# Performance work log

Hardware: AMD Instinct MI355X
Metric: run time of the kernel (lower is better)

The kernel has to match this reference:

```python
import jax, jax.numpy as jnp
import numpy as np

B, L, D, H = 4, 2048, 1024, 16
HD = D // H
EPS = 1e-5


def _layernorm(x, g, b):
    mu = jnp.mean(x, axis=-1, keepdims=True)
    var = jnp.mean(jnp.square(x - mu), axis=-1, keepdims=True)
    return (x - mu) * jax.lax.rsqrt(var + EPS) * g + b


def _rotate_half(x):
    x1, x2 = jnp.split(x, 2, axis=-1)
    return jnp.concatenate([-x2, x1], axis=-1)


def setup_inputs() -> dict:
    key = jax.random.key(0)
    ks = jax.random.split(key, 12)
    s = 0.02
    return {
        "x": jax.random.normal(ks[0], (B, L, D), jnp.float32),
        "pos_cos": jax.random.uniform(ks[1], (B, L, D), jnp.float32),
        "pos_sin": jax.random.uniform(ks[2], (B, L, D), jnp.float32),
        "attn_mask": jnp.zeros((B, L), jnp.float32),
        "Wq": jax.random.normal(ks[3], (D, D), jnp.float32) * s,
        "Wk": jax.random.normal(ks[4], (D, D), jnp.float32) * s,
        "Wv": jax.random.normal(ks[5], (D, D), jnp.float32) * s,
        "Wo": jax.random.normal(ks[6], (D, D), jnp.float32) * s,
        "W1": jax.random.normal(ks[7], (D, 2 * D), jnp.float32) * s,
        "W2": jax.random.normal(ks[8], (D, D), jnp.float32) * s,
        "g1": jnp.ones((D,), jnp.float32),
        "b1": jnp.zeros((D,), jnp.float32),
        "g2": jnp.ones((D,), jnp.float32),
        "b2": jnp.zeros((D,), jnp.float32),
    }


def reference(x, pos_cos, pos_sin, attn_mask, Wq, Wk, Wv, Wo, W1, W2, g1, b1, g2, b2):
    # --- attention sublayer (pre-LN) ---
    residual = x
    xn = _layernorm(x, g1, b1)
    split_heads = lambda t: t.reshape(B, L, H, HD).transpose(0, 2, 1, 3)  # [B,H,L,hd]
    q = split_heads(xn @ Wq)
    k = split_heads(xn @ Wk)
    v = split_heads(xn @ Wv)
    cos = split_heads(pos_cos)
    sin = split_heads(pos_sin)
    q = q * cos + _rotate_half(q) * sin
    k = k * cos + _rotate_half(k) * sin
    scores = jnp.einsum('bhqd,bhkd->bhqk', q, k) / np.float32(np.sqrt(HD))
    scores = scores + attn_mask[:, None, None, :]  # additive mask over keys
    probs = jax.nn.softmax(scores, axis=-1)
    ctx = jnp.einsum('bhqk,bhkd->bhqd', probs, v)
    ctx = ctx.transpose(0, 2, 1, 3).reshape(B, L, D)
    x = residual + ctx @ Wo
    # --- SwiGLU FFN sublayer (pre-LN) ---
    residual = x
    xn = _layernorm(x, g2, b2)
    h = xn @ W1
    x1, x2 = h[..., :D], h[..., D:]
    ffn = (jax.nn.silu(x1) * x2) @ W2
    return residual + ffn
```

## Files before the change

kernel.cpp:

```cpp
#include <hip/hip_runtime.h>
#include <hip/hip_bf16.h>

typedef unsigned short ushort_t;
typedef short short8 __attribute__((ext_vector_type(8)));
typedef unsigned short u16x4 __attribute__((ext_vector_type(4)));
typedef float f32x4 __attribute__((ext_vector_type(4)));
typedef int int2v __attribute__((ext_vector_type(2)));
typedef int int4v __attribute__((ext_vector_type(4)));

#define MFMA_BF16 __builtin_amdgcn_mfma_f32_16x16x32_bf16

#define GLDS16(g, l) __builtin_amdgcn_global_load_lds( \
    (__attribute__((address_space(1))) void*)(g), \
    (__attribute__((address_space(3))) void*)(l), 16, 0, 0)

__device__ __forceinline__ unsigned short f2bf(float f) {
  union { float f; unsigned u; } v; v.f = f;
  unsigned r = v.u + 0x7FFFu + ((v.u >> 16) & 1u);
  return (unsigned short)(r >> 16);
}
__device__ __forceinline__ float bf2f(unsigned short h) {
  union { unsigned u; float f; } v; v.u = ((unsigned)h) << 16;
  return v.f;
}
__device__ __forceinline__ unsigned pack_bf2(float a, float b) {
  __hip_bfloat162 t = __float22bfloat162_rn(float2{a, b});
  union { __hip_bfloat162 h; unsigned u; } v; v.h = t;
  return v.u;
}
__device__ __forceinline__ float exp2_raw(float x) {
  float r;
  asm volatile("v_exp_f32 %0, %1" : "=v"(r) : "v"(x));
  return r;
}

#define BB 4
#define LL 2048
#define DD 1024
#define HH 16
#define HD 64
#define NROW (BB * LL)
#define LOG2E 1.4426950408889634f

template <int PERM>
__global__ __launch_bounds__(256) void wconv(const float* __restrict__ W,
                                             ushort_t* __restrict__ WT,
                                             int R, int C) {
  __shared__ float tile[32][33];
  const int ct = blockIdx.x * 32, rt = blockIdx.y * 32;
  const int tx = threadIdx.x & 31, ty = threadIdx.x >> 5;
#pragma unroll
  for (int j = 0; j < 4; ++j)
    tile[ty + j * 8][tx] = W[(size_t)(rt + ty + j * 8) * C + ct + tx];
  __syncthreads();
  int orow0 = ct;
  if (PERM)
    orow0 = (ct < 1024) ? ((ct >> 5) * 64) : ((((ct - 1024) >> 5) * 64) + 32);
#pragma unroll
  for (int j = 0; j < 4; ++j)
    WT[(size_t)(orow0 + ty + j * 8) * R + rt + tx] = f2bf(tile[tx][ty + j * 8]);
}

__global__ void mask_scale(const float* __restrict__ mask,
                           float* __restrict__ maskl) {
  const int i = blockIdx.x * 256 + threadIdx.x;
  maskl[i] = mask[i] * LOG2E;
}

template <int BIN>
__global__ __launch_bounds__(256) void ln_kernel(const void* __restrict__ xin,
                                                 const float* __restrict__ g,
                                                 const float* __restrict__ bt,
                                                 ushort_t* __restrict__ out,
                                                 ushort_t* __restrict__ xb) {
  const int row = blockIdx.x, t = threadIdx.x;
  f32x4 v;
  if (BIN) {
    const u16x4 hv =
        *(const u16x4*)((const ushort_t*)xin + (size_t)row * DD + t * 4);
    v[0] = bf2f(hv[0]); v[1] = bf2f(hv[1]);
    v[2] = bf2f(hv[2]); v[3] = bf2f(hv[3]);
  } else {
    v = *(const f32x4*)((const float*)xin + (size_t)row * DD + t * 4);
    if (xb) {
      u16x4 xo;
      xo[0] = f2bf(v[0]); xo[1] = f2bf(v[1]);
      xo[2] = f2bf(v[2]); xo[3] = f2bf(v[3]);
      *(u16x4*)(xb + (size_t)row * DD + t * 4) = xo;
    }
  }
  float s = v[0] + v[1] + v[2] + v[3];
  float sq = v[0] * v[0] + v[1] * v[1] + v[2] * v[2] + v[3] * v[3];
#pragma unroll
  for (int off = 1; off < 64; off <<= 1) {
    s += __shfl_xor(s, off);
    sq += __shfl_xor(sq, off);
  }
  __shared__ float aw[4], aq[4];
  if ((t & 63) == 0) { aw[t >> 6] = s; aq[t >> 6] = sq; }
  __syncthreads();
  s = aw[0] + aw[1] + aw[2] + aw[3];
  sq = aq[0] + aq[1] + aq[2] + aq[3];
  const float mu = s * (1.f / DD);
  const float var = sq * (1.f / DD) - mu * mu;
  const float rs = rsqrtf(var + 1e-5f);
  u16x4 o;
#pragma unroll
  for (int j = 0; j < 4; ++j) {
    const int c = t * 4 + j;
    o[j] = f2bf((v[j] - mu) * rs * g[c] + bt[c]);
  }
  *(u16x4*)(out + (size_t)row * DD + t * 4) = o;
}

template <int EPI>
__global__ __launch_bounds__(256) void gemm64(
    const ushort_t* __restrict__ A, const ushort_t* __restrict__ BT,
    const float* __restrict__ pcos, const float* __restrict__ psin,
    ushort_t* __restrict__ qh, ushort_t* __restrict__ kh,
    ushort_t* __restrict__ vt, ushort_t* __restrict__ gact,
    ushort_t* __restrict__ Cb, float* __restrict__ Cf,
    const ushort_t* __restrict__ residb,
    int M, int N, int K) {
  __shared__ ushort_t As[128 * 64];
  __shared__ ushort_t Bs[128 * 64];
  const int tid = threadIdx.x;
  const int lane = tid & 63;
  const int w = tid >> 6;
  const int wr = w >> 1, wc = w & 1;
  const int orig = blockIdx.y * gridDim.x + blockIdx.x;
  const int xcd = orig & 7;
  const int lid = orig >> 3;
  const int bm = (xcd * 8 + (lid & 7)) * 128;
  const int bn = (lid >> 3) * 128;
  const int fr = lane & 15;
  const int hi = lane >> 4;
  const int srow8 = lane >> 3;
  const int schunk = (lane & 7) ^ srow8;
  f32x4 acc[4][4];
#pragma unroll
  for (int m = 0; m < 4; ++m)
#pragma unroll
    for (int n = 0; n < 4; ++n) acc[m][n] = (f32x4){0.f, 0.f, 0.f, 0.f};

  const int nk = K >> 6;
  for (int kt = 0; kt < nk; ++kt) {
    __syncthreads();
#pragma unroll
    for (int c = 0; c < 4; ++c) {
      const int rbase = w * 32 + c * 8;
      const int grow = rbase + srow8;
      GLDS16(A + (size_t)(bm + grow) * K + kt * 64 + schunk * 8,
             &As[rbase * 64]);
      GLDS16(BT + (size_t)(bn + grow) * K + kt * 64 + schunk * 8,
             &Bs[rbase * 64]);
    }
    asm volatile("s_waitcnt vmcnt(0)" ::: "memory");
    __syncthreads();
#pragma unroll
    for (int khf = 0; khf < 2; ++khf) {
      short8 af[4], bf_[4];
#pragma unroll
      for (int m = 0; m < 4; ++m) {
        const int r = wr * 64 + m * 16 + fr;
        af[m] = *(const short8*)&As[r * 64 + (((khf << 2) + hi) ^ (fr & 7)) * 8];
      }
#pragma unroll
      for (int n = 0; n < 4; ++n) {
        const int r = wc * 64 + n * 16 + fr;
        bf_[n] = *(const short8*)&Bs[r * 64 + (((khf << 2) + hi) ^ (fr & 7)) * 8];
      }
#pragma unroll
      for (int m = 0; m < 4; ++m)
#pragma unroll
        for (int n = 0; n < 4; ++n)
          acc[m][n] = MFMA_BF16(af[m], bf_[n], acc[m][n], 0, 0, 0);
    }
  }

  if (EPI == 1) {
    const int gcol = bn + wc * 64;
    const int region = gcol >> 10;
    const int h = (gcol & 1023) >> 6;
    const int b = bm >> 11;
    if (region < 2) {
      const float qs = (region == 0) ? (0.125f * LOG2E) : 1.0f;
      ushort_t* dstbuf = (region == 0) ? qh : kh;
      const int dbase = h * 64;
#pragma unroll
      for (int m = 0; m < 4; ++m) {
        const int gr0 = bm + wr * 64 + m * 16 + hi * 4;
#pragma unroll
        for (int r = 0; r < 4; ++r) {
          const int gr = gr0 + r;
          const int l = gr & 2047;
          const float* pcr = pcos + (size_t)gr * DD + dbase;
          const float* psr = psin + (size_t)gr * DD + dbase;
          ushort_t* dst = dstbuf + ((size_t)(b * HH + h) * LL + l) * HD;
#pragma unroll
          for (int n = 0; n < 2; ++n) {
            const int dlo = n * 16 + fr;
            const float xlo = acc[m][n][r], xhi = acc[m][n + 2][r];
            dst[dlo] = f2bf((xlo * pcr[dlo] - xhi * psr[dlo]) * qs);
            dst[dlo + 32] = f2bf((xhi * pcr[dlo + 32] + xlo * psr[dlo + 32]) * qs);
          }
        }
      }
    } else {
      const size_t bhv = (size_t)(b * HH + h);
      const int l0 = (bm & 2047) + wr * 64;
      const int lt = l0 >> 6;
#pragma unroll
      for (int m = 0; m < 4; ++m) {
        const int slotb = 32 * (m >> 1) + 8 * hi + 4 * (m & 1);
#pragma unroll
        for (int n = 0; n < 4; ++n) {
          const int hd = n * 16 + fr;
          u16x4 wv;
          wv[0] = f2bf(acc[m][n][0]);
          wv[1] = f2bf(acc[m][n][1]);
          wv[2] = f2bf(acc[m][n][2]);
          wv[3] = f2bf(acc[m][n][3]);
          *(u16x4*)(vt + (bhv * HD + hd) * LL + lt * 64 + slotb) = wv;
        }
      }
    }
  } else if (EPI == 2) {
    const int jbase = ((bn + wc * 64) >> 6) * 32;
#pragma unroll
    for (int m = 0; m < 4; ++m) {
      const int gr0 = bm + wr * 64 + m * 16 + hi * 4;
#pragma unroll
      for (int r = 0; r < 4; ++r) {
        ushort_t* dst = gact + (size_t)(gr0 + r) * DD + jbase;
#pragma unroll
        for (int n = 0; n < 2; ++n) {
          const float x1 = acc[m][n][r];
          const float x2 = acc[m][n + 2][r];
          dst[n * 16 + fr] = f2bf(x1 / (1.f + __expf(-x1)) * x2);
        }
      }
    }
  } else {
#pragma unroll
    for (int m = 0; m < 4; ++m)
#pragma unroll
      for (int n = 0; n < 4; ++n)
#pragma unroll
        for (int r = 0; r < 4; ++r) {
          const int gr = bm + wr * 64 + m * 16 + hi * 4 + r;
          const int gc = bn + wc * 64 + n * 16 + fr;
          const size_t o = (size_t)gr * N + gc;
          if (EPI == 3) Cb[o] = f2bf(bf2f(residb[o]) + acc[m][n][r]);
          else          Cf[o] = bf2f(residb[o]) + acc[m][n][r];
        }
  }
}

__global__ __launch_bounds__(512) void attn_kernel(
    const ushort_t* __restrict__ qh, const ushort_t* __restrict__ kh,
    const ushort_t* __restrict__ vt, const float* __restrict__ maskl,
    ushort_t* __restrict__ ctx) {
  const int tid = threadIdx.x, lane = tid & 63, w = tid >> 6;
  const int flat = blockIdx.y * gridDim.x + blockIdx.x;
  const int xcd = flat & 7;
  const int slot = flat >> 3;
  const int bh = xcd * 8 + (slot >> 4);
  const int q0 = (slot & 15) * 128;
  const int b = bh >> 4, h = bh & 15;
  __shared__ ushort_t Ks[2][64 * 64];
  __shared__ ushort_t Vs[2][64 * 64];
  const int fr = lane & 15;
  const int hi = lane >> 4;
  const int fo = hi * 8;
  const int qrow = q0 + w * 16 + fr;
  const size_t qoff = ((size_t)bh * LL + qrow) * HD + fo;
  const short8 qf0 = *(const short8*)(qh + qoff);
  const short8 qf1 = *(const short8*)(qh + qoff + 32);
  short8 ones;
#pragma unroll
  for (int i = 0; i < 8; ++i) ones[i] = (short)0x3F80;

  f32x4 oacc[4];
  f32x4 lacc = (f32x4){0.f, 0.f, 0.f, 0.f};
#pragma unroll
  for (int m = 0; m < 4; ++m) oacc[m] = (f32x4){0.f, 0.f, 0.f, 0.f};

  const int lrow = lane >> 3;
  const int lcs = ((lane & 7) ^ lrow) * 8;
  const int rr = w * 8 + lrow;

  const float* mrow = maskl + (size_t)b * LL;

  const int NT = LL / 128;
  for (int kt = 0; kt < NT; ++kt) {
    __syncthreads();
    GLDS16(kh + ((size_t)bh * LL + kt * 128 + rr) * HD + lcs, &Ks[0][w * 512]);
    GLDS16(kh + ((size_t)bh * LL + kt * 128 + 64 + rr) * HD + lcs,
           &Ks[1][w * 512]);
    GLDS16(vt + ((size_t)bh * HD + rr) * LL + kt * 128 + lcs, &Vs[0][w * 512]);
    GLDS16(vt + ((size_t)bh * HD + rr) * LL + kt * 128 + 64 + lcs,
           &Vs[1][w * 512]);
    f32x4 mk[8];
#pragma unroll
    for (int n = 0; n < 8; ++n)
      mk[n] = *(const f32x4*)(mrow + kt * 128 + n * 16 + hi * 4);
    asm volatile("s_waitcnt vmcnt(0)" ::: "memory");
    __syncthreads();

#pragma unroll
    for (int sub = 0; sub < 2; ++sub) {
      f32x4 s[4];
#pragma unroll
      for (int n = 0; n < 4; ++n) s[n] = mk[sub * 4 + n];
      __builtin_amdgcn_s_setprio(1);
#pragma unroll
      for (int n = 0; n < 4; ++n) {
        const int krow = n * 16 + fr;
#pragma unroll
        for (int c = 0; c < 2; ++c) {
          const int col = (c * 32 + fo) ^ ((fr & 7) * 8);
          const short8 kf = *(const short8*)&Ks[sub][krow * 64 + col];
          s[n] = MFMA_BF16(kf, c ? qf1 : qf0, s[n], 0, 0, 0);
        }
      }
      __builtin_amdgcn_s_setprio(0);
      unsigned pk[4][2];
#pragma unroll
      for (int n = 0; n < 4; ++n) {
        const float p0 = exp2_raw(s[n][0]);
        const float p1 = exp2_raw(s[n][1]);
        const float p2 = exp2_raw(s[n][2]);
        const float p3 = exp2_raw(s[n][3]);
        pk[n][0] = pack_bf2(p0, p1);
        pk[n][1] = pack_bf2(p2, p3);
      }
      __builtin_amdgcn_s_setprio(1);
#pragma unroll
      for (int c = 0; c < 2; ++c) {
        int4v pw = {(int)pk[2 * c][0], (int)pk[2 * c][1],
                    (int)pk[2 * c + 1][0], (int)pk[2 * c + 1][1]};
        union { int4v i; short8 s; } pf; pf.i = pw;
#pragma unroll
        for (int m = 0; m < 4; ++m) {
          const int row = m * 16 + fr;
          const int col = (c * 32 + fo) ^ ((fr & 7) * 8);
          const short8 vf = *(const short8*)&Vs[sub][row * 64 + col];
          oacc[m] = MFMA_BF16(vf, pf.s, oacc[m], 0, 0, 0);
        }
        lacc = MFMA_BF16(ones, pf.s, lacc, 0, 0, 0);
      }
      __builtin_amdgcn_s_setprio(0);
    }
  }
  const float inv = 1.f / lacc[0];
  const int q = q0 + w * 16 + fr;
  ushort_t* dst = ctx + ((size_t)b * LL + q) * DD + h * 64 + hi * 4;
#pragma unroll
  for (int m = 0; m < 4; ++m) {
    int2v val;
    val[0] = (int)pack_bf2(oacc[m][0] * inv, oacc[m][1] * inv);
    val[1] = (int)pack_bf2(oacc[m][2] * inv, oacc[m][3] * inv);
    *(int2v*)(dst + m * 16) = val;
  }
}

extern "C" void kernel_launch(void* const* d_in, const int* in_sizes, int n_in,
                              void* d_out, int out_size, void* d_ws,
                              size_t ws_size, hipStream_t stream) {
  const float* x = (const float*)d_in[0];
  const float* pcos = (const float*)d_in[1];
  const float* psin = (const float*)d_in[2];
  const float* mask = (const float*)d_in[3];
  const float* Wq = (const float*)d_in[4];
  const float* Wk = (const float*)d_in[5];
  const float* Wv = (const float*)d_in[6];
  const float* Wo = (const float*)d_in[7];
  const float* W1 = (const float*)d_in[8];
  const float* W2 = (const float*)d_in[9];
  const float* g1 = (const float*)d_in[10];
  const float* b1 = (const float*)d_in[11];
  const float* g2 = (const float*)d_in[12];
  const float* b2 = (const float*)d_in[13];
  float* out = (float*)d_out;
  char* ws = (char*)d_ws;

  ushort_t* WQKVT = (ushort_t*)(ws);
  ushort_t* WOT = (ushort_t*)(ws + 6291456);
  ushort_t* W1T = (ushort_t*)(ws + 8388608);
  ushort_t* W2T = (ushort_t*)(ws + 12582912);
  ushort_t* XN = (ushort_t*)(ws + 14680064);
  float* MASKL = (float*)(ws + 31457280);
  ushort_t* XB = (ushort_t*)(ws + 31457280 + 1048576);
  ushort_t* GACT = (ushort_t*)(ws + 31457280 + 33554432);
  ushort_t* QH = (ushort_t*)(ws + 81788928);
  ushort_t* KH = (ushort_t*)(ws + 98566144);
  ushort_t* VT = (ushort_t*)(ws + 115343360);
  ushort_t* CTX = (ushort_t*)(ws + 132120576);
  ushort_t* XMIDB = (ushort_t*)(ws + 148897792);

  wconv<0><<<dim3(32, 32), 256, 0, stream>>>(Wq, WQKVT, 1024, 1024);
  wconv<0><<<dim3(32, 32), 256, 0, stream>>>(Wk, WQKVT + 1024 * 1024, 1024, 1024);
  wconv<0><<<dim3(32, 32), 256, 0, stream>>>(Wv, WQKVT + 2 * 1024 * 1024, 1024, 1024);
  wconv<0><<<dim3(32, 32), 256, 0, stream>>>(Wo, WOT, 1024, 1024);
  wconv<1><<<dim3(64, 32), 256, 0, stream>>>(W1, W1T, 1024, 2048);
  wconv<0><<<dim3(32, 32), 256, 0, stream>>>(W2, W2T, 1024, 1024);
  mask_scale<<<(BB * LL) / 256, 256, 0, stream>>>(mask, MASKL);

  ln_kernel<0><<<NROW, 256, 0, stream>>>(x, g1, b1, XN, XB);
  gemm64<1><<<dim3(24, 64), 256, 0, stream>>>(
      XN, WQKVT, pcos, psin, QH, KH, VT, nullptr, nullptr, nullptr, nullptr,
      NROW, 3072, 1024);
  attn_kernel<<<dim3(16, 64), 512, 0, stream>>>(QH, KH, VT, MASKL, CTX);
  gemm64<3><<<dim3(8, 64), 256, 0, stream>>>(
      CTX, WOT, nullptr, nullptr, nullptr, nullptr, nullptr, nullptr, XMIDB,
      nullptr, XB, NROW, 1024, 1024);
  ln_kernel<1><<<NROW, 256, 0, stream>>>(XMIDB, g2, b2, XN, nullptr);
  gemm64<2><<<dim3(16, 64), 256, 0, stream>>>(
      XN, W1T, nullptr, nullptr, nullptr, nullptr, nullptr, GACT, nullptr,
      nullptr, nullptr, NROW, 2048, 1024);
  gemm64<4><<<dim3(8, 64), 256, 0, stream>>>(
      GACT, W2T, nullptr, nullptr, nullptr, nullptr, nullptr, nullptr, nullptr,
      out, XMIDB, NROW, 1024, 1024);
}
```

Baseline: 333.5 us.

## Double-buffer LDS tiles in gemm64 to overlap global loads with MFMA

Splits the A/B shared-memory tiles into two buffers and issues the global-to-LDS loads for the next K tile before computing on the current one. A partial vmcnt wait lets the prefetch stay in flight while the current tile is consumed. It also raises wave priority around the MFMA block. This doubles LDS use per block to 64KB, which may lower occupancy, and adds a barrier at the end of each iteration.

```diff
diff --git a/kernel.cpp b/kernel.cpp
--- a/kernel.cpp
+++ b/kernel.cpp
@@ -122,8 +122,8 @@
     ushort_t* __restrict__ Cb, float* __restrict__ Cf,
     const ushort_t* __restrict__ residb,
     int M, int N, int K) {
-  __shared__ ushort_t As[128 * 64];
-  __shared__ ushort_t Bs[128 * 64];
+  __shared__ ushort_t As[2][128 * 64];
+  __shared__ ushort_t Bs[2][128 * 64];
   const int tid = threadIdx.x;
   const int lane = tid & 63;
   const int w = tid >> 6;
@@ -143,19 +143,29 @@
 #pragma unroll
     for (int n = 0; n < 4; ++n) acc[m][n] = (f32x4){0.f, 0.f, 0.f, 0.f};
 
+#define STAGE64(kt, bb)                                                      \
+  {                                                                          \
+    _Pragma("unroll") for (int c = 0; c < 4; ++c) {                          \
+      const int rbase = w * 32 + c * 8;                                      \
+      const int grow = rbase + srow8;                                        \
+      GLDS16(A + (size_t)(bm + grow) * K + (kt) * 64 + schunk * 8,           \
+             &As[bb][rbase * 64]);                                           \
+      GLDS16(BT + (size_t)(bn + grow) * K + (kt) * 64 + schunk * 8,          \
+             &Bs[bb][rbase * 64]);                                           \
+    }                                                                        \
+  }
+
   const int nk = K >> 6;
+  STAGE64(0, 0);
+#pragma unroll 1
   for (int kt = 0; kt < nk; ++kt) {
-    __syncthreads();
-#pragma unroll
-    for (int c = 0; c < 4; ++c) {
-      const int rbase = w * 32 + c * 8;
-      const int grow = rbase + srow8;
-      GLDS16(A + (size_t)(bm + grow) * K + kt * 64 + schunk * 8,
-             &As[rbase * 64]);
-      GLDS16(BT + (size_t)(bn + grow) * K + kt * 64 + schunk * 8,
-             &Bs[rbase * 64]);
-    }
-    asm volatile("s_waitcnt vmcnt(0)" ::: "memory");
+    const int cur = kt & 1;
+    if (kt + 1 < nk) {
+      STAGE64(kt + 1, cur ^ 1);
+      asm volatile("s_waitcnt vmcnt(8)" ::: "memory");
+    } else {
+      asm volatile("s_waitcnt vmcnt(0)" ::: "memory");
+    }
     __syncthreads();
 #pragma unroll
     for (int khf = 0; khf < 2; ++khf) {
@@ -163,20 +173,26 @@
 #pragma unroll
       for (int m = 0; m < 4; ++m) {
         const int r = wr * 64 + m * 16 + fr;
-        af[m] = *(const short8*)&As[r * 64 + (((khf << 2) + hi) ^ (fr & 7)) * 8];
+        af[m] =
+            *(const short8*)&As[cur][r * 64 + (((khf << 2) + hi) ^ (fr & 7)) * 8];
       }
 #pragma unroll
       for (int n = 0; n < 4; ++n) {
         const int r = wc * 64 + n * 16 + fr;
-        bf_[n] = *(const short8*)&Bs[r * 64 + (((khf << 2) + hi) ^ (fr & 7)) * 8];
-      }
+        bf_[n] =
+            *(const short8*)&Bs[cur][r * 64 + (((khf << 2) + hi) ^ (fr & 7)) * 8];
+      }
+      __builtin_amdgcn_s_setprio(1);
 #pragma unroll
       for (int m = 0; m < 4; ++m)
 #pragma unroll
         for (int n = 0; n < 4; ++n)
           acc[m][n] = MFMA_BF16(af[m], bf_[n], acc[m][n], 0, 0, 0);
-    }
-  }
+      __builtin_amdgcn_s_setprio(0);
+    }
+    __syncthreads();
+  }
+#undef STAGE64
 
   if (EPI == 1) {
     const int gcol = bn + wc * 64;
```

New measurement: 320.2 us (median of 2 runs). -4.0%, faster.
